# Kernel optimization log

Hardware: AMD Instinct MI355X
Metric: run time of the kernel (lower is better)

## Reference

```python
import jax, jax.numpy as jnp
import numpy as np

N = 50000      # nodes
E = 800000     # edges
IN = 64        # in_channels
HID = 128      # hidden_channels
HEADS = 4
D = HID // HEADS  # 32 per-head dim
G = 64         # graphs in batch


def setup_inputs() -> dict:
    key = jax.random.key(0)
    ks = jax.random.split(key, 24)
    def p(k, shape):
        return (jax.random.normal(k, shape, jnp.float32) * 0.05)
    x = jax.random.normal(ks[0], (N, IN), jnp.float32)
    edge_index = jax.random.randint(ks[1], (2, E), 0, N, dtype=jnp.int32).astype(jnp.int64)
    batch = jnp.sort(jax.random.randint(ks[2], (N,), 0, G, dtype=jnp.int32)).astype(jnp.int64)
    inp = {"x": x, "edge_index": edge_index, "batch": batch}
    # layer 1: in -> HID (heads*D), with root/skip projection
    inp["Wq1"] = p(ks[3], (IN, HID)); inp["bq1"] = p(ks[4], (HID,))
    inp["Wk1"] = p(ks[5], (IN, HID)); inp["bk1"] = p(ks[6], (HID,))
    inp["Wv1"] = p(ks[7], (IN, HID)); inp["bv1"] = p(ks[8], (HID,))
    inp["Ws1"] = p(ks[9], (IN, HID)); inp["bs1"] = p(ks[10], (HID,))
    # layer 2: HID -> HID
    inp["Wq2"] = p(ks[11], (HID, HID)); inp["bq2"] = p(ks[12], (HID,))
    inp["Wk2"] = p(ks[13], (HID, HID)); inp["bk2"] = p(ks[14], (HID,))
    inp["Wv2"] = p(ks[15], (HID, HID)); inp["bv2"] = p(ks[16], (HID,))
    inp["Ws2"] = p(ks[17], (HID, HID)); inp["bs2"] = p(ks[18], (HID,))
    # readout linear HID -> 2
    inp["Wl"] = p(ks[19], (HID, 2)); inp["bl"] = p(ks[20], (2,))
    return inp


def transformer_conv(x, src, dst, Wq, bq, Wk, bk, Wv, bv, Ws, bs):
    """PyG TransformerConv (concat=True, root_weight=True, beta=False, eval mode)."""
    n = x.shape[0]
    q = (x @ Wq + bq).reshape(n, HEADS, D)
    k = (x @ Wk + bk).reshape(n, HEADS, D)
    v = (x @ Wv + bv).reshape(n, HEADS, D)
    # per-edge attention logits: query at target (dst), key/value at source (src)
    qi, kj, vj = q[dst], k[src], v[src]           # [E, H, D]
    logits = jnp.sum(qi * kj, axis=-1) / jnp.sqrt(jnp.asarray(D, x.dtype))  # [E, H]
    # segment softmax over incoming edges of each target node
    m = jax.ops.segment_max(logits, dst, num_segments=n)   # [N, H]
    p = jnp.exp(logits - m[dst])                           # [E, H]
    s = jax.ops.segment_sum(p, dst, num_segments=n)        # [N, H]
    alpha = p / s[dst]                                     # [E, H]
    agg = jax.ops.segment_sum(alpha[..., None] * vj, dst, num_segments=n)  # [N, H, D]
    out = agg.reshape(n, HID) + (x @ Ws + bs)              # concat heads + skip
    return out


def reference(x, edge_index, batch,
              Wq1, bq1, Wk1, bk1, Wv1, bv1, Ws1, bs1,
              Wq2, bq2, Wk2, bk2, Wv2, bv2, Ws2, bs2,
              Wl, bl):
    src, dst = edge_index[0], edge_index[1]
    h = jax.nn.relu(transformer_conv(x, src, dst, Wq1, bq1, Wk1, bk1, Wv1, bv1, Ws1, bs1))
    h = jax.nn.relu(transformer_conv(h, src, dst, Wq2, bq2, Wk2, bk2, Wv2, bv2, Ws2, bs2))
    # global mean pool per graph
    counts = jax.ops.segment_sum(jnp.ones((h.shape[0],), h.dtype), batch, num_segments=G)
    pooled = jax.ops.segment_sum(h, batch, num_segments=G) / jnp.maximum(counts, 1.0)[:, None]
    return pooled @ Wl + bl  # [G, 2]
```

## Files before the change

### kernel.cpp

```cpp
#include <hip/hip_runtime.h>
#include <hip/hip_bf16.h>
#include <cstdint>
#include <cstddef>

#define N_NODES 50000
#define N_EDGES 800000
#define IN_CH 64
#define HID_CH 128
#define N_GRAPHS 64

#define NB_SCAN ((N_NODES + 255) / 256)
#define NB_CNT4 ((N_EDGES + 1023) / 1024)
#define NB_GEMM ((N_NODES + 63) / 64)
#define W_ELEMS (4 * IN_CH * 128 + 4 * HID_CH * 128)
#define NB_CONV ((W_ELEMS + 255) / 256)

typedef short s16x8 __attribute__((ext_vector_type(8)));
typedef float f32x4 __attribute__((ext_vector_type(4)));
typedef float f32x2 __attribute__((ext_vector_type(2)));

__device__ __forceinline__ float bf2f(__hip_bfloat16 v) { return __bfloat162float(v); }
__device__ __forceinline__ float bfbits2f(unsigned hs) {
  union { unsigned u; float f; } v; v.u = hs << 16; return v.f;
}
__device__ __forceinline__ float bfhi2f(unsigned w) {
  union { unsigned u; float f; } v; v.u = w & 0xffff0000u; return v.f;
}
__device__ __forceinline__ short f2bfs(float f) {
  __hip_bfloat16 h = __float2bfloat16(f); return *(short*)&h;
}
__device__ __forceinline__ unsigned short f2bfu(float f) {
  __hip_bfloat16 h = __float2bfloat16(f); return *(unsigned short*)&h;
}
__device__ __forceinline__ int clamp_id(int v) {
  if (v < 0) v = 0;
  if (v >= N_NODES) v = N_NODES - 1;
  return v;
}

__device__ __forceinline__ unsigned char f2fp8(float v) {
  return (unsigned char)(__builtin_amdgcn_cvt_pk_fp8_f32(v, v, 0, false) & 0xff);
}
template<bool HI>
__device__ __forceinline__ f32x2 fp8pair(unsigned w) {
  return __builtin_amdgcn_cvt_pk_f32_fp8(w, HI);
}

__global__ __launch_bounds__(256)
void prep(const int* __restrict__ ei, int* __restrict__ cnt,
          unsigned short* __restrict__ rank,
          const float* __restrict__ w1q, const float* __restrict__ w1k,
          const float* __restrict__ w1v, const float* __restrict__ w1s,
          const float* __restrict__ w2q, const float* __restrict__ w2k,
          const float* __restrict__ w2v, const float* __restrict__ w2s,
          __hip_bfloat16* d1q, __hip_bfloat16* d1k, __hip_bfloat16* d1v, __hip_bfloat16* d1s,
          __hip_bfloat16* d2q, __hip_bfloat16* d2k, __hip_bfloat16* d2v, __hip_bfloat16* d2s)
{
  int bx = blockIdx.x;
  if (bx < NB_CNT4) {
    int e0 = bx * 1024 + threadIdx.x * 4;
    if (e0 >= N_EDGES) return;
    if (e0 + 3 < N_EDGES) {
      int4 dv = *(const int4*)(ei + N_EDGES + e0);
      unsigned short r0 = (unsigned short)atomicAdd(&cnt[clamp_id(dv.x)], 1);
      unsigned short r1 = (unsigned short)atomicAdd(&cnt[clamp_id(dv.y)], 1);
      unsigned short r2 = (unsigned short)atomicAdd(&cnt[clamp_id(dv.z)], 1);
      unsigned short r3 = (unsigned short)atomicAdd(&cnt[clamp_id(dv.w)], 1);
      ushort4 rv; rv.x = r0; rv.y = r1; rv.z = r2; rv.w = r3;
      *(ushort4*)(rank + e0) = rv;
    } else {
      for (int j = 0; j < 4; ++j)
        if (e0 + j < N_EDGES)
          rank[e0 + j] = (unsigned short)atomicAdd(&cnt[clamp_id(ei[N_EDGES + e0 + j])], 1);
    }
    return;
  }
  int j = (bx - NB_CNT4) * 256 + threadIdx.x;
  if (j >= W_ELEMS) return;
  const float* S[8] = {w1q, w1k, w1v, w1s, w2q, w2k, w2v, w2s};
  __hip_bfloat16* D[8] = {d1q, d1k, d1v, d1s, d2q, d2k, d2v, d2s};
  int m, r;
  if (j < 4 * IN_CH * 128) { m = j >> 13; r = j & 8191; }
  else { int jj = j - 4 * IN_CH * 128; m = 4 + (jj >> 14); r = jj & 16383; }
  int k = r >> 7, c = r & 127;
  D[m][(((k >> 3) * 128 + c) << 3) + (k & 7)] = __float2bfloat16(S[m][r]);
}

template<int KD, int XF32>
__device__ __forceinline__ void gemm_body(
    int bg, const void* X,
    const short* __restrict__ WTq, const short* __restrict__ WTk,
    const short* __restrict__ WTv, const short* __restrict__ WTs,
    const float* __restrict__ bq, const float* __restrict__ bk,
    const float* __restrict__ bv, const float* __restrict__ bs,
    short* Qo, unsigned char* KV8, short* So, short* lds)
{
  constexpr int KT = KD / 32;
  constexpr int CHUNKS = KD * 16;
  const int tid  = threadIdx.x;
  const int wid  = tid >> 6;
  const int lane = tid & 63;
  const int quad = lane >> 4;
  const int mm   = lane & 15;
  const int rt   = wid & 1;
  const int ch   = wid >> 1;
  const int rowbase = bg * 64 + rt * 32;

  s16x8 afrag[2][KT];
  #pragma unroll
  for (int t = 0; t < 2; ++t) {
    const int arow = rowbase + t * 16 + mm;
    if (arow < N_NODES) {
      if (XF32) {
        const float* xp = (const float*)X + (size_t)arow * KD;
        #pragma unroll
        for (int kt = 0; kt < KT; ++kt) {
          const float4* p = (const float4*)(xp + kt * 32 + quad * 8);
          float4 a = p[0], b = p[1];
          s16x8 fr;
          fr[0] = f2bfs(a.x); fr[1] = f2bfs(a.y); fr[2] = f2bfs(a.z); fr[3] = f2bfs(a.w);
          fr[4] = f2bfs(b.x); fr[5] = f2bfs(b.y); fr[6] = f2bfs(b.z); fr[7] = f2bfs(b.w);
          afrag[t][kt] = fr;
        }
      } else {
        const short* xp = (const short*)X + (size_t)arow * KD;
        #pragma unroll
        for (int kt = 0; kt < KT; ++kt)
          afrag[t][kt] = *(const s16x8*)(xp + kt * 32 + quad * 8);
      }
    } else {
      #pragma unroll
      for (int kt = 0; kt < KT; ++kt)
        afrag[t][kt] = (s16x8){0,0,0,0,0,0,0,0};
    }
  }

  const short* wts[4] = {WTq, WTk, WTv, WTs};
  const float* bias[4] = {bq, bk, bv, bs};

  #pragma unroll
  for (int mat = 0; mat < 4; ++mat) {
    if (mat > 0) __syncthreads();
    {
      const uint4* src = (const uint4*)wts[mat];
      uint4* dst = (uint4*)lds;
      #pragma unroll
      for (int i = 0; i < CHUNKS / 256; ++i)
        dst[tid + i * 256] = src[tid + i * 256];
    }
    __syncthreads();

    f32x4 acc[4][2];
    #pragma unroll
    for (int c4 = 0; c4 < 4; ++c4) {
      float b = bias[mat][ch * 64 + c4 * 16 + mm];
      f32x4 av = {b, b, b, b};
      acc[c4][0] = av; acc[c4][1] = av;
    }
    #pragma unroll
    for (int kt = 0; kt < KT; ++kt) {
      #pragma unroll
      for (int c4 = 0; c4 < 4; ++c4) {
        s16x8 bfrag = *(const s16x8*)(lds + ((((kt * 4 + quad) << 7) + ch * 64 + c4 * 16 + mm) << 3));
        acc[c4][0] = __builtin_amdgcn_mfma_f32_16x16x32_bf16(afrag[0][kt], bfrag, acc[c4][0], 0, 0, 0);
        acc[c4][1] = __builtin_amdgcn_mfma_f32_16x16x32_bf16(afrag[1][kt], bfrag, acc[c4][1], 0, 0, 0);
      }
    }
    if (mat == 1 || mat == 2) {
      unsigned char* O8 = KV8 + ((mat == 1) ? 0 : 128);
      #pragma unroll
      for (int c4 = 0; c4 < 4; ++c4) {
        const int col = ch * 64 + c4 * 16 + mm;
        #pragma unroll
        for (int t = 0; t < 2; ++t) {
          #pragma unroll
          for (int r = 0; r < 4; ++r) {
            int row = rowbase + t * 16 + quad * 4 + r;
            if (row < N_NODES)
              O8[(size_t)row * 256 + col] = f2fp8(acc[c4][t][r]);
          }
        }
      }
    } else {
      short* O = (mat == 0) ? Qo : So;
      #pragma unroll
      for (int c4 = 0; c4 < 4; ++c4) {
        const int col = ch * 64 + c4 * 16 + mm;
        #pragma unroll
        for (int t = 0; t < 2; ++t) {
          #pragma unroll
          for (int r = 0; r < 4; ++r) {
            int row = rowbase + t * 16 + quad * 4 + r;
            if (row < N_NODES)
              ((__hip_bfloat16*)O)[(size_t)row * 128 + col] = __float2bfloat16(acc[c4][t][r]);
          }
        }
      }
    }
  }
}

__global__ __launch_bounds__(256)
void scan1(const int* __restrict__ cnt, int* __restrict__ offs, int* __restrict__ bsum) {
  __shared__ int wsum[4];
  int t = threadIdx.x, lane = t & 63, w = t >> 6;
  int i = blockIdx.x * 256 + t;
  int v = (i < N_NODES) ? cnt[i] : 0;
  int x = v;
  #pragma unroll
  for (int o = 1; o < 64; o <<= 1) { int y = __shfl_up(x, o, 64); if (lane >= o) x += y; }
  if (lane == 63) wsum[w] = x;
  __syncthreads();
  if (t == 0) {
    int run = 0;
    #pragma unroll
    for (int k = 0; k < 4; ++k) { int tv = wsum[k]; wsum[k] = run; run += tv; }
    bsum[blockIdx.x] = run;
  }
  __syncthreads();
  if (i <= N_NODES) offs[i] = wsum[w] + x - v;
}

__global__ __launch_bounds__(256)
void scan2(int* __restrict__ bsum) {
  __shared__ int wsum[4];
  int t = threadIdx.x, lane = t & 63, w = t >> 6;
  int v = (t < NB_SCAN) ? bsum[t] : 0;
  int x = v;
  #pragma unroll
  for (int o = 1; o < 64; o <<= 1) { int y = __shfl_up(x, o, 64); if (lane >= o) x += y; }
  if (lane == 63) wsum[w] = x;
  __syncthreads();
  if (t == 0) {
    int run = 0;
    #pragma unroll
    for (int k = 0; k < 4; ++k) { int tv = wsum[k]; wsum[k] = run; run += tv; }
  }
  __syncthreads();
  if (t < NB_SCAN) bsum[t] = wsum[w] + x - v;
}

__global__ __launch_bounds__(256)
void scatter_gemm1(const int* __restrict__ ei, const int* __restrict__ offs,
                   const int* __restrict__ bsum, const unsigned short* __restrict__ rank,
                   int* __restrict__ ssrc,
                   const float* __restrict__ X,
                   const short* __restrict__ w1q, const short* __restrict__ w1k,
                   const short* __restrict__ w1v, const short* __restrict__ w1s,
                   const float* __restrict__ b1q, const float* __restrict__ b1k,
                   const float* __restrict__ b1v, const float* __restrict__ b1s,
                   short* Qb, unsigned char* KV8, short* Sb)
{
  __shared__ short lds[IN_CH * 128];
  int bx = blockIdx.x;
  if (bx >= NB_GEMM) {
    int e0 = (bx - NB_GEMM) * 1024 + threadIdx.x * 4;
    if (e0 >= N_EDGES) return;
    if (e0 + 3 < N_EDGES) {
      int4 sv = *(const int4*)(ei + e0);
      int4 dv = *(const int4*)(ei + N_EDGES + e0);
      ushort4 rv = *(const ushort4*)(rank + e0);
      int d0 = clamp_id(dv.x), d1 = clamp_id(dv.y);
      int d2 = clamp_id(dv.z), d3 = clamp_id(dv.w);
      int p0 = offs[d0] + bsum[d0 >> 8] + rv.x;
      int p1 = offs[d1] + bsum[d1 >> 8] + rv.y;
      int p2 = offs[d2] + bsum[d2 >> 8] + rv.z;
      int p3 = offs[d3] + bsum[d3 >> 8] + rv.w;
      ssrc[p0] = clamp_id(sv.x);
      ssrc[p1] = clamp_id(sv.y);
      ssrc[p2] = clamp_id(sv.z);
      ssrc[p3] = clamp_id(sv.w);
    } else {
      for (int j = 0; j < 4; ++j) {
        int e = e0 + j;
        if (e < N_EDGES) {
          int src = clamp_id(ei[e]);
          int dst = clamp_id(ei[N_EDGES + e]);
          ssrc[offs[dst] + bsum[dst >> 8] + rank[e]] = src;
        }
      }
    }
    return;
  }
  gemm_body<IN_CH, 1>(bx, X, w1q, w1k, w1v, w1s, b1q, b1k, b1v, b1s,
                      Qb, KV8, Sb, lds);
}

__global__ __launch_bounds__(256)
void attn_kernel(const unsigned short* __restrict__ Q, const unsigned char* __restrict__ KV8,
                 const unsigned short* S,
                 const int* __restrict__ offs, const int* __restrict__ bsum,
                 const int* __restrict__ ssrc, unsigned short* H)
{
  const int dst = blockIdx.x * 4 + (threadIdx.x >> 6);
  if (dst >= N_NODES) return;
  const int lane = threadIdx.x & 63;
  const int sub  = lane >> 4;
  const int cl   = lane & 15;

  const float qs = 0.17677669529663687f * 1.4426950408889634f;
  uint4 qw = *(const uint4*)(Q + (size_t)dst * 128 + cl * 8);
  float q[8], a[8];
  #pragma unroll
  for (int i = 0; i < 4; ++i) {
    unsigned w = ((unsigned*)&qw)[i];
    q[2 * i]     = bfbits2f(w & 0xffffu) * qs;
    q[2 * i + 1] = bfhi2f(w) * qs;
    a[2 * i] = 0.f; a[2 * i + 1] = 0.f;
  }
  float s = 0.f;

  const int e0 = offs[dst] + bsum[dst >> 8];
  const int e1 = offs[dst + 1] + bsum[(dst + 1) >> 8];
  const int iters = (e1 - e0 + 3) >> 2;

  if (iters > 0) {
    int e = e0 + sub;
    bool have = (e < e1);
    int src = have ? ssrc[e] : ssrc[e0];
    float ph = have ? 1.f : 0.f;
    const unsigned char* kvp = KV8 + (size_t)src * 256 + cl * 8;
    uint2 kw = *(const uint2*)(kvp);
    uint2 vw = *(const uint2*)(kvp + 128);

    for (int it = 0; it < iters; ++it) {
      uint2 kwn, vwn;
      int en = e + 4;
      bool haven = (en < e1);
      float phn = haven ? 1.f : 0.f;
      if (it + 1 < iters) {
        int srcn = haven ? ssrc[en] : ssrc[e0];
        const unsigned char* kvn = KV8 + (size_t)srcn * 256 + cl * 8;
        kwn = *(const uint2*)(kvn);
        vwn = *(const uint2*)(kvn + 128);
      } else {
        kwn = kw; vwn = vw;
      }
      f32x2 k0 = fp8pair<false>(kw.x), k1 = fp8pair<true>(kw.x);
      f32x2 k2 = fp8pair<false>(kw.y), k3 = fp8pair<true>(kw.y);
      float d = q[0] * k0.x + q[1] * k0.y + q[2] * k1.x + q[3] * k1.y
              + q[4] * k2.x + q[5] * k2.y + q[6] * k3.x + q[7] * k3.y;
      d += __shfl_xor(d, 1, 64);
      d += __shfl_xor(d, 2, 64);
      float p = exp2f(d) * ph;
      s += p;
      f32x2 v0 = fp8pair<false>(vw.x), v1 = fp8pair<true>(vw.x);
      f32x2 v2 = fp8pair<false>(vw.y), v3 = fp8pair<true>(vw.y);
      a[0] += p * v0.x; a[1] += p * v0.y;
      a[2] += p * v1.x; a[3] += p * v1.y;
      a[4] += p * v2.x; a[5] += p * v2.y;
      a[6] += p * v3.x; a[7] += p * v3.y;
      kw = kwn; vw = vwn; ph = phn; e = en;
    }
  }

  s += __shfl_xor(s, 16, 64);
  s += __shfl_xor(s, 32, 64);
  #pragma unroll
  for (int i = 0; i < 8; ++i) {
    a[i] += __shfl_xor(a[i], 16, 64);
    a[i] += __shfl_xor(a[i], 32, 64);
  }
  const float inv = (s > 0.f) ? (1.0f / s) : 0.f;

  if (sub == 0) {
    uint4 sw = *(const uint4*)(S + (size_t)dst * 128 + cl * 8);
    uint4 ow;
    #pragma unroll
    for (int i = 0; i < 4; ++i) {
      unsigned w = ((unsigned*)&sw)[i];
      float o0 = fmaxf(a[2 * i] * inv     + bfbits2f(w & 0xffffu), 0.f);
      float o1 = fmaxf(a[2 * i + 1] * inv + bfhi2f(w), 0.f);
      ((unsigned*)&ow)[i] = (unsigned)f2bfu(o0) | ((unsigned)f2bfu(o1) << 16);
    }
    *(uint4*)(H + (size_t)dst * 128 + cl * 8) = ow;
  }
}

__global__ __launch_bounds__(256)
void gemm2(const short* __restrict__ X,
           const short* __restrict__ w2q, const short* __restrict__ w2k,
           const short* __restrict__ w2v, const short* __restrict__ w2s,
           const float* __restrict__ b2q, const float* __restrict__ b2k,
           const float* __restrict__ b2v, const float* __restrict__ b2s,
           short* Qb, unsigned char* KV8, short* Sb)
{
  __shared__ short lds[HID_CH * 128];
  gemm_body<HID_CH, 0>(blockIdx.x, X, w2q, w2k, w2v, w2s, b2q, b2k, b2v, b2s,
                       Qb, KV8, Sb, lds);
}

__device__ __forceinline__ int lower_bound_i(const int* __restrict__ b, int n, int val) {
  int lo = 0, hi = n;
  while (lo < hi) { int mid = (lo + hi) >> 1; if (b[mid] < val) lo = mid + 1; else hi = mid; }
  return lo;
}

__global__ __launch_bounds__(128)
void pool_partial(const __hip_bfloat16* __restrict__ H, const int* __restrict__ batch,
                  float* __restrict__ pooled)
{
  const int g = blockIdx.x >> 4, p = blockIdx.x & 15, t = threadIdx.x;
  const int s = lower_bound_i(batch, N_NODES, g);
  const int e = lower_bound_i(batch, N_NODES, g + 1);
  const int len = e - s;
  if (len <= 0) return;
  const int chunk = (len + 15) >> 4;
  const int a = s + p * chunk;
  const int b = min(a + chunk, e);
  if (a >= b) return;
  float sum = 0.f;
  for (int i = a; i < b; ++i) sum += bf2f(H[(size_t)i * 128 + t]);
  atomicAdd(&pooled[g * 128 + t], sum);
}

__global__ __launch_bounds__(128)
void pool_final(const float* __restrict__ pooled, const int* __restrict__ batch,
                const float* __restrict__ Wl, const float* __restrict__ bl,
                float* __restrict__ out)
{
  const int g = blockIdx.x, t = threadIdx.x;
  __shared__ float r0[128], r1[128];
  const int s = lower_bound_i(batch, N_NODES, g);
  const int e = lower_bound_i(batch, N_NODES, g + 1);
  const float inv = 1.0f / (float)max(e - s, 1);
  const float pc = pooled[g * 128 + t] * inv;
  r0[t] = pc * Wl[t * 2 + 0];
  r1[t] = pc * Wl[t * 2 + 1];
  __syncthreads();
  for (int o = 64; o > 0; o >>= 1) {
    if (t < o) { r0[t] += r0[t + o]; r1[t] += r1[t + o]; }
    __syncthreads();
  }
  if (t == 0) {
    out[g * 2 + 0] = r0[0] + bl[0];
    out[g * 2 + 1] = r1[0] + bl[1];
  }
}


extern "C" void kernel_launch(void* const* d_in, const int* in_sizes, int n_in,
                              void* d_out, int out_size, void* d_ws, size_t ws_size,
                              hipStream_t stream) {
  uintptr_t base = (uintptr_t)d_ws;
  auto take = [&](size_t bytes) -> uintptr_t {
    uintptr_t p = base;
    base += (bytes + 255) & ~(size_t)255;
    return p;
  };

  int*   cnt    = (int*)take((size_t)N_NODES * 4);
  float* pooled = (float*)take((size_t)N_GRAPHS * 128 * 4);
  int*   offs   = (int*)take((size_t)(N_NODES + 1) * 4);
  int*   bsum   = (int*)take((size_t)NB_SCAN * 4);
  int*   ssrc   = (int*)take((size_t)N_EDGES * 4);
  unsigned short* rank = (unsigned short*)take((size_t)N_EDGES * 2);
  short* Qb     = (short*)take((size_t)N_NODES * 128 * 2);
  unsigned char* KV8 = (unsigned char*)take((size_t)N_NODES * 256);
  short* Sb     = (short*)take((size_t)N_NODES * 128 * 2);
  short* wt1q   = (short*)take((size_t)IN_CH * 128 * 2);
  short* wt1k   = (short*)take((size_t)IN_CH * 128 * 2);
  short* wt1v   = (short*)take((size_t)IN_CH * 128 * 2);
  short* wt1s   = (short*)take((size_t)IN_CH * 128 * 2);
  short* wt2q   = (short*)take((size_t)HID_CH * 128 * 2);
  short* wt2k   = (short*)take((size_t)HID_CH * 128 * 2);
  short* wt2v   = (short*)take((size_t)HID_CH * 128 * 2);
  short* wt2s   = (short*)take((size_t)HID_CH * 128 * 2);

  const int* ei    = (const int*)d_in[1];
  const int* batch = (const int*)d_in[2];

  size_t zspan = (size_t)((char*)pooled + (size_t)N_GRAPHS * 128 * 4 - (char*)cnt);
  hipMemsetAsync(cnt, 0, zspan, stream);

  prep<<<NB_CNT4 + NB_CONV, 256, 0, stream>>>(
      ei, cnt, rank,
      (const float*)d_in[3], (const float*)d_in[5], (const float*)d_in[7], (const float*)d_in[9],
      (const float*)d_in[11], (const float*)d_in[13], (const float*)d_in[15], (const float*)d_in[17],
      (__hip_bfloat16*)wt1q, (__hip_bfloat16*)wt1k, (__hip_bfloat16*)wt1v, (__hip_bfloat16*)wt1s,
      (__hip_bfloat16*)wt2q, (__hip_bfloat16*)wt2k, (__hip_bfloat16*)wt2v, (__hip_bfloat16*)wt2s);

  scan1<<<NB_SCAN, 256, 0, stream>>>(cnt, offs, bsum);
  scan2<<<1, 256, 0, stream>>>(bsum);

  scatter_gemm1<<<NB_GEMM + NB_CNT4, 256, 0, stream>>>(
      ei, offs, bsum, rank, ssrc,
      (const float*)d_in[0],
      wt1q, wt1k, wt1v, wt1s,
      (const float*)d_in[4], (const float*)d_in[6], (const float*)d_in[8], (const float*)d_in[10],
      Qb, KV8, Sb);

  const int attn_grid = (N_NODES + 3) / 4;

  attn_kernel<<<attn_grid, 256, 0, stream>>>(
      (const unsigned short*)Qb, KV8,
      (const unsigned short*)Sb, offs, bsum, ssrc, (unsigned short*)Sb);

  gemm2<<<NB_GEMM, 256, 0, stream>>>(
      Sb, wt2q, wt2k, wt2v, wt2s,
      (const float*)d_in[12], (const float*)d_in[14], (const float*)d_in[16], (const float*)d_in[18],
      Qb, KV8, Sb);

  attn_kernel<<<attn_grid, 256, 0, stream>>>(
      (const unsigned short*)Qb, KV8,
      (const unsigned short*)Sb, offs, bsum, ssrc, (unsigned short*)Sb);

  pool_partial<<<N_GRAPHS * 16, 128, 0, stream>>>(
      (const __hip_bfloat16*)Sb, batch, pooled);
  pool_final<<<N_GRAPHS, 128, 0, stream>>>(pooled, batch, (const float*)d_in[19],
                                           (const float*)d_in[20], (float*)d_out);
}
```

Measured before the change: 294.0 us.

## Split node-projection GEMMs across four blocks per row tile, one weight matrix each

Each 64-row GEMM tile used to loop over the Q, K, V and skip weight matrices inside one block. It is now split into four blocks, each handling one matrix, so there are four times as many blocks and no intra-block reload/sync loop. Because the layer-2 GEMM blocks run concurrently and read the same input, the skip output now goes to a separate buffer (Sb2) instead of overwriting the input in place. The cost is that each block reloads the A tile, roughly quadrupling activation reads.

New measurement: 305.9 us. 1.04x slower.

```diff
diff --git a/kernel.cpp b/kernel.cpp
--- a/kernel.cpp
+++ b/kernel.cpp
@@ -12,6 +12,7 @@
 #define NB_SCAN ((N_NODES + 255) / 256)
 #define NB_CNT4 ((N_EDGES + 1023) / 1024)
 #define NB_GEMM ((N_NODES + 63) / 64)
+#define NB_GEMM4 (NB_GEMM * 4)
 #define W_ELEMS (4 * IN_CH * 128 + 4 * HID_CH * 128)
 #define NB_CONV ((W_ELEMS + 255) / 256)
 
@@ -87,12 +88,9 @@
 }
 
 template<int KD, int XF32>
-__device__ __forceinline__ void gemm_body(
-    int bg, const void* X,
-    const short* __restrict__ WTq, const short* __restrict__ WTk,
-    const short* __restrict__ WTv, const short* __restrict__ WTs,
-    const float* __restrict__ bq, const float* __restrict__ bk,
-    const float* __restrict__ bv, const float* __restrict__ bs,
+__device__ __forceinline__ void gemm_body_onemat(
+    int bg, int mat, const void* X,
+    const short* __restrict__ WT, const float* __restrict__ bias,
     short* Qo, unsigned char* KV8, short* So, short* lds)
 {
   constexpr int KT = KD / 32;
@@ -105,6 +103,14 @@
   const int rt   = wid & 1;
   const int ch   = wid >> 1;
   const int rowbase = bg * 64 + rt * 32;
+
+  {
+    const uint4* src = (const uint4*)WT;
+    uint4* dst = (uint4*)lds;
+    #pragma unroll
+    for (int i = 0; i < CHUNKS / 256; ++i)
+      dst[tid + i * 256] = src[tid + i * 256];
+  }
 
   s16x8 afrag[2][KT];
   #pragma unroll
@@ -135,65 +141,52 @@
     }
   }
 
-  const short* wts[4] = {WTq, WTk, WTv, WTs};
-  const float* bias[4] = {bq, bk, bv, bs};
-
-  #pragma unroll
-  for (int mat = 0; mat < 4; ++mat) {
-    if (mat > 0) __syncthreads();
-    {
-      const uint4* src = (const uint4*)wts[mat];
-      uint4* dst = (uint4*)lds;
+  __syncthreads();
+
+  f32x4 acc[4][2];
+  #pragma unroll
+  for (int c4 = 0; c4 < 4; ++c4) {
+    float b = bias[ch * 64 + c4 * 16 + mm];
+    f32x4 av = {b, b, b, b};
+    acc[c4][0] = av; acc[c4][1] = av;
+  }
+  #pragma unroll
+  for (int kt = 0; kt < KT; ++kt) {
+    #pragma unroll
+    for (int c4 = 0; c4 < 4; ++c4) {
+      s16x8 bfrag = *(const s16x8*)(lds + ((((kt * 4 + quad) << 7) + ch * 64 + c4 * 16 + mm) << 3));
+      acc[c4][0] = __builtin_amdgcn_mfma_f32_16x16x32_bf16(afrag[0][kt], bfrag, acc[c4][0], 0, 0, 0);
+      acc[c4][1] = __builtin_amdgcn_mfma_f32_16x16x32_bf16(afrag[1][kt], bfrag, acc[c4][1], 0, 0, 0);
+    }
+  }
+
+  if (mat == 1 || mat == 2) {
+    unsigned char* O8 = KV8 + ((mat == 1) ? 0 : 128);
+    #pragma unroll
+    for (int c4 = 0; c4 < 4; ++c4) {
+      const int col = ch * 64 + c4 * 16 + mm;
       #pragma unroll
-      for (int i = 0; i < CHUNKS / 256; ++i)
-        dst[tid + i * 256] = src[tid + i * 256];
-    }
-    __syncthreads();
-
-    f32x4 acc[4][2];
-    #pragma unroll
-    for (int c4 = 0; c4 < 4; ++c4) {
-      float b = bias[mat][ch * 64 + c4 * 16 + mm];
-      f32x4 av = {b, b, b, b};
-      acc[c4][0] = av; acc[c4][1] = av;
-    }
-    #pragma unroll
-    for (int kt = 0; kt < KT; ++kt) {
-      #pragma unroll
-      for (int c4 = 0; c4 < 4; ++c4) {
-        s16x8 bfrag = *(const s16x8*)(lds + ((((kt * 4 + quad) << 7) + ch * 64 + c4 * 16 + mm) << 3));
-        acc[c4][0] = __builtin_amdgcn_mfma_f32_16x16x32_bf16(afrag[0][kt], bfrag, acc[c4][0], 0, 0, 0);
-        acc[c4][1] = __builtin_amdgcn_mfma_f32_16x16x32_bf16(afrag[1][kt], bfrag, acc[c4][1], 0, 0, 0);
-      }
-    }
-    if (mat == 1 || mat == 2) {
-      unsigned char* O8 = KV8 + ((mat == 1) ? 0 : 128);
-      #pragma unroll
-      for (int c4 = 0; c4 < 4; ++c4) {
-        const int col = ch * 64 + c4 * 16 + mm;
+      for (int t = 0; t < 2; ++t) {
         #pragma unroll
-        for (int t = 0; t < 2; ++t) {
-          #pragma unroll
-          for (int r = 0; r < 4; ++r) {
-            int row = rowbase + t * 16 + quad * 4 + r;
-            if (row < N_NODES)
-              O8[(size_t)row * 256 + col] = f2fp8(acc[c4][t][r]);
-          }
+        for (int r = 0; r < 4; ++r) {
+          int row = rowbase + t * 16 + quad * 4 + r;
+          if (row < N_NODES)
+            O8[(size_t)row * 256 + col] = f2fp8(acc[c4][t][r]);
         }
       }
-    } else {
-      short* O = (mat == 0) ? Qo : So;
+    }
+  } else {
+    short* O = (mat == 0) ? Qo : So;
+    #pragma unroll
+    for (int c4 = 0; c4 < 4; ++c4) {
+      const int col = ch * 64 + c4 * 16 + mm;
       #pragma unroll
-      for (int c4 = 0; c4 < 4; ++c4) {
-        const int col = ch * 64 + c4 * 16 + mm;
+      for (int t = 0; t < 2; ++t) {
         #pragma unroll
-        for (int t = 0; t < 2; ++t) {
-          #pragma unroll
-          for (int r = 0; r < 4; ++r) {
-            int row = rowbase + t * 16 + quad * 4 + r;
-            if (row < N_NODES)
-              ((__hip_bfloat16*)O)[(size_t)row * 128 + col] = __float2bfloat16(acc[c4][t][r]);
-          }
+        for (int r = 0; r < 4; ++r) {
+          int row = rowbase + t * 16 + quad * 4 + r;
+          if (row < N_NODES)
+            ((__hip_bfloat16*)O)[(size_t)row * 128 + col] = __float2bfloat16(acc[c4][t][r]);
         }
       }
     }
@@ -253,8 +246,8 @@
 {
   __shared__ short lds[IN_CH * 128];
   int bx = blockIdx.x;
-  if (bx >= NB_GEMM) {
-    int e0 = (bx - NB_GEMM) * 1024 + threadIdx.x * 4;
+  if (bx >= NB_GEMM4) {
+    int e0 = (bx - NB_GEMM4) * 1024 + threadIdx.x * 4;
     if (e0 >= N_EDGES) return;
     if (e0 + 3 < N_EDGES) {
       int4 sv = *(const int4*)(ei + e0);
@@ -282,8 +275,11 @@
     }
     return;
   }
-  gemm_body<IN_CH, 1>(bx, X, w1q, w1k, w1v, w1s, b1q, b1k, b1v, b1s,
-                      Qb, KV8, Sb, lds);
+  const int bg  = bx >> 2;
+  const int mat = bx & 3;
+  const short* wts[4] = {w1q, w1k, w1v, w1s};
+  const float* bias[4] = {b1q, b1k, b1v, b1s};
+  gemm_body_onemat<IN_CH, 1>(bg, mat, X, wts[mat], bias[mat], Qb, KV8, Sb, lds);
 }
 
 __global__ __launch_bounds__(256)
@@ -383,11 +379,14 @@
            const short* __restrict__ w2v, const short* __restrict__ w2s,
            const float* __restrict__ b2q, const float* __restrict__ b2k,
            const float* __restrict__ b2v, const float* __restrict__ b2s,
-           short* Qb, unsigned char* KV8, short* Sb)
+           short* Qb, unsigned char* KV8, short* Sb2)
 {
   __shared__ short lds[HID_CH * 128];
-  gemm_body<HID_CH, 0>(blockIdx.x, X, w2q, w2k, w2v, w2s, b2q, b2k, b2v, b2s,
-                       Qb, KV8, Sb, lds);
+  const int bg  = blockIdx.x >> 2;
+  const int mat = blockIdx.x & 3;
+  const short* wts[4] = {w2q, w2k, w2v, w2s};
+  const float* bias[4] = {b2q, b2k, b2v, b2s};
+  gemm_body_onemat<HID_CH, 0>(bg, mat, X, wts[mat], bias[mat], Qb, KV8, Sb2, lds);
 }
 
 __device__ __forceinline__ int lower_bound_i(const int* __restrict__ b, int n, int val) {
@@ -458,6 +457,7 @@
   short* Qb     = (short*)take((size_t)N_NODES * 128 * 2);
   unsigned char* KV8 = (unsigned char*)take((size_t)N_NODES * 256);
   short* Sb     = (short*)take((size_t)N_NODES * 128 * 2);
+  short* Sb2    = (short*)take((size_t)N_NODES * 128 * 2);
   short* wt1q   = (short*)take((size_t)IN_CH * 128 * 2);
   short* wt1k   = (short*)take((size_t)IN_CH * 128 * 2);
   short* wt1v   = (short*)take((size_t)IN_CH * 128 * 2);
@@ -483,7 +483,7 @@
   scan1<<<NB_SCAN, 256, 0, stream>>>(cnt, offs, bsum);
   scan2<<<1, 256, 0, stream>>>(bsum);
 
-  scatter_gemm1<<<NB_GEMM + NB_CNT4, 256, 0, stream>>>(
+  scatter_gemm1<<<NB_GEMM4 + NB_CNT4, 256, 0, stream>>>(
       ei, offs, bsum, rank, ssrc,
       (const float*)d_in[0],
       wt1q, wt1k, wt1v, wt1s,
@@ -496,17 +496,17 @@
       (const unsigned short*)Qb, KV8,
       (const unsigned short*)Sb, offs, bsum, ssrc, (unsigned short*)Sb);
 
-  gemm2<<<NB_GEMM, 256, 0, stream>>>(
+  gemm2<<<NB_GEMM4, 256, 0, stream>>>(
       Sb, wt2q, wt2k, wt2v, wt2s,
       (const float*)d_in[12], (const float*)d_in[14], (const float*)d_in[16], (const float*)d_in[18],
-      Qb, KV8, Sb);
+      Qb, KV8, Sb2);
 
   attn_kernel<<<attn_grid, 256, 0, stream>>>(
       (const unsigned short*)Qb, KV8,
-      (const unsigned short*)Sb, offs, bsum, ssrc, (unsigned short*)Sb);
+      (const unsigned short*)Sb2, offs, bsum, ssrc, (unsigned short*)Sb2);
 
   pool_partial<<<N_GRAPHS * 16, 128, 0, stream>>>(
-      (const __hip_bfloat16*)Sb, batch, pooled);
+      (const __hip_bfloat16*)Sb2, batch, pooled);
   pool_final<<<N_GRAPHS, 128, 0, stream>>>(pooled, batch, (const float*)d_in[19],
                                            (const float*)d_in[20], (float*)d_out);
 }
```
